# Kernel optimization log

Hardware: AMD Instinct MI355X
Metric: run time of the kernel (lower is better)

The kernel has to match this reference:

```python
import jax, jax.numpy as jnp
import numpy as np

N = 100000        # nodes
E_HALF = 1600000  # directed edges before symmetrization
NFEAT, NHID, NOUT = 512, 256, 64
K = 10            # Chebyshev order


def setup_inputs() -> dict:
    key = jax.random.key(0)
    k_feat, k_src, k_dst, k_w1, k_w2, k_tmp = jax.random.split(key, 6)
    feature = jax.random.normal(k_feat, (N, NFEAT), jnp.float32)
    src = jax.random.randint(k_src, (E_HALF,), 0, N, jnp.int32)
    dst = jax.random.randint(k_dst, (E_HALF,), 0, N, jnp.int32)
    # symmetrize so the adjacency (and hence the normalized Laplacian) is symmetric
    edge_index = jnp.stack([jnp.concatenate([src, dst]), jnp.concatenate([dst, src])])  # [2, 2*E_HALF]
    W1 = jax.random.normal(k_w1, (NHID, NFEAT), jnp.float32) / np.sqrt(NFEAT)
    b1 = jnp.zeros((NHID,), jnp.float32)
    W2 = jax.random.normal(k_w2, (NOUT, NHID), jnp.float32) / np.sqrt(NHID)
    b2 = jnp.zeros((NOUT,), jnp.float32)
    # ChebnetII_prop.temp is initialized to 1.0; jitter so relu/grads are non-trivial
    temp = 1.0 + 0.1 * jax.random.normal(k_tmp, (K + 1,), jnp.float32)
    return {"feature": feature, "W1": W1, "b1": b1, "W2": W2, "b2": b2,
            "temp": temp, "edge_index": edge_index}


def _cheb_coeffs(temp):
    # coe[i] = 2/(K+1) * sum_j relu(temp)[j] * T_i(x_j),  x_j = cos((K-j+0.5)*pi/(K+1))
    # and T_i(cos(theta)) = cos(i*theta)
    coe_tmp = jax.nn.relu(temp)
    j = jnp.arange(K + 1, dtype=temp.dtype)
    theta = (K - j + 0.5) * jnp.pi / (K + 1)          # [K+1]
    i = jnp.arange(K + 1, dtype=temp.dtype)
    T = jnp.cos(i[:, None] * theta[None, :])           # [K+1, K+1] Chebyshev eval table
    return (2.0 / (K + 1)) * (T @ coe_tmp)             # [K+1]


def reference(feature, W1, b1, W2, b2, temp, edge_index):
    # dense MLP part (dropout is identity in eval mode)
    x = jax.nn.relu(feature @ W1.T + b1)               # [N, NHID]
    x = x @ W2.T + b2                                  # [N, NOUT]

    # ChebnetII_prop: propagate with L_tilde = L_sym - I = -D^{-1/2} A D^{-1/2}
    row, col = edge_index[0], edge_index[1]
    w = jnp.ones(row.shape, x.dtype)                   # unit edge weights (binary adjacency)
    deg = jax.ops.segment_sum(w, row, num_segments=N)  # [N]
    dinv = jnp.where(deg > 0, jax.lax.rsqrt(jnp.maximum(deg, 1.0)), 0.0)
    norm = -dinv[row] * w * dinv[col]                  # [E] edge weights of (L - I)

    def prop(v):  # v: [N, NOUT] -> (L - I) @ v via gather/scatter
        return jax.ops.segment_sum(norm[:, None] * v[col], row, num_segments=N)

    coe = _cheb_coeffs(temp)
    Tx0 = x
    Tx1 = prop(x)
    out = coe[0] / 2.0 * Tx0 + coe[1] * Tx1
    for i in range(2, K + 1):                          # Chebyshev recursion (K fixed, small)
        Tx2 = 2.0 * prop(Tx1) - Tx0
        out = out + coe[i] * Tx2
        Tx0, Tx1 = Tx1, Tx2
    return out                                         # [N, NOUT]
```

## Files before the change

kernel.cpp:

```cpp
#include <hip/hip_runtime.h>

#define K_ORDER 10
#define NFEAT 512
#define NHID 256
#define NOUT 64
#define PI_F 3.14159265358979323846f
#define SCAN_CHUNK 2048

typedef __bf16 bf16x8 __attribute__((ext_vector_type(8)));
typedef unsigned short ushort8 __attribute__((ext_vector_type(8)));
typedef float f32x4 __attribute__((ext_vector_type(4)));

__device__ __forceinline__ float bf2f(unsigned short u) {
    union { unsigned int i; float f; } x;
    x.i = ((unsigned int)u) << 16;
    return x.f;
}

__global__ void detect_kernel(const unsigned short* __restrict__ temp, int* __restrict__ flag) {
    if (threadIdx.x == 0 && blockIdx.x == 0) {
        int cnt = 0;
        for (int i = 0; i < K_ORDER + 1; ++i) {
            unsigned short s = temp[i];
            if (s >= 0x3E00 && s < 0x4080) cnt++;
        }
        flag[0] = (cnt >= 9) ? 1 : 0;
    }
}


__global__ void count_deg_kernel(const int* __restrict__ row, int* __restrict__ deg, int e) {
    int i = blockIdx.x * blockDim.x + threadIdx.x;
    if (i < e) atomicAdd(&deg[row[i]], 1);
}

__global__ void dinv_kernel(const int* __restrict__ deg, float* __restrict__ dinv, int n) {
    int i = blockIdx.x * blockDim.x + threadIdx.x;
    if (i < n) {
        int d = deg[i];
        dinv[i] = (d > 0) ? rsqrtf((float)d) : 0.0f;
    }
}


__global__ __launch_bounds__(256) void partial_sum_kernel(const int* __restrict__ deg,
                                                          int* __restrict__ bsum, int n) {
    __shared__ int ws[4];
    int b = blockIdx.x, t = threadIdx.x;
    int base = b * SCAN_CHUNK + t * 8;
    int s = 0;
    #pragma unroll
    for (int j = 0; j < 8; ++j) { int i = base + j; if (i < n) s += deg[i]; }
    #pragma unroll
    for (int m = 1; m < 64; m <<= 1) s += __shfl_xor(s, m, 64);
    if ((t & 63) == 0) ws[t >> 6] = s;
    __syncthreads();
    if (t == 0) bsum[b] = ws[0] + ws[1] + ws[2] + ws[3];
}

__global__ void scan_small_kernel(const int* __restrict__ bsum, int* __restrict__ boff,
                                  int* __restrict__ rowptr, int nb, int n) {
    int t = threadIdx.x;
    int v = (t < nb) ? bsum[t] : 0;
    int x = v;
    #pragma unroll
    for (int m = 1; m < 64; m <<= 1) { int y = __shfl_up(x, m, 64); if (t >= m) x += y; }
    if (t < nb) boff[t] = x - v;
    if (t == 63) rowptr[n] = x;
}

__global__ __launch_bounds__(256) void scan_apply_kernel(const int* __restrict__ deg,
                                                         const int* __restrict__ boff,
                                                         int* __restrict__ rowptr,
                                                         int* __restrict__ cursor, int n) {
    __shared__ int wtot[4];
    __shared__ int woff_s[4];
    int b = blockIdx.x, t = threadIdx.x;
    int lane = t & 63, wid = t >> 6;
    int base = b * SCAN_CHUNK + t * 8;
    int v[8], s[8];
    int run = 0;
    #pragma unroll
    for (int j = 0; j < 8; ++j) {
        int i = base + j;
        v[j] = (i < n) ? deg[i] : 0;
        run += v[j];
        s[j] = run;
    }
    int tsum = run;
    int x = tsum;
    #pragma unroll
    for (int m = 1; m < 64; m <<= 1) { int y = __shfl_up(x, m, 64); if (lane >= m) x += y; }
    int texcl = x - tsum;
    if (lane == 63) wtot[wid] = x;
    __syncthreads();
    if (t == 0) {
        int r = 0;
        #pragma unroll
        for (int w = 0; w < 4; ++w) { woff_s[w] = r; r += wtot[w]; }
    }
    __syncthreads();
    int ebase = boff[b] + woff_s[wid] + texcl;
    #pragma unroll
    for (int j = 0; j < 8; ++j) {
        int i = base + j;
        if (i < n) { int ex = ebase + s[j] - v[j]; rowptr[i] = ex; cursor[i] = ex; }
    }
}

__global__ void scatter_kernel(const int* __restrict__ row, const int* __restrict__ col,
                               int* __restrict__ cursor, int* __restrict__ cols_s, int e) {
    int i = blockIdx.x * blockDim.x + threadIdx.x;
    if (i < e) {
        int p = atomicAdd(&cursor[row[i]], 1);
        cols_s[p] = col[i];
    }
}


__global__ void coef_kernel(const void* __restrict__ temp, const int* __restrict__ flag,
                            float* __restrict__ coe) {
    int i = threadIdx.x;
    bool isbf = flag[0] != 0;
    if (i <= K_ORDER) {
        float s = 0.0f;
        #pragma unroll
        for (int j = 0; j <= K_ORDER; ++j) {
            float t = isbf ? bf2f(((const unsigned short*)temp)[j]) : ((const float*)temp)[j];
            t = fmaxf(t, 0.0f);
            float theta = ((float)(K_ORDER - j) + 0.5f) * PI_F / (float)(K_ORDER + 1);
            s += cosf((float)i * theta) * t;
        }
        coe[i] = (2.0f / (float)(K_ORDER + 1)) * s;
    }
}


template<int BN, bool RELU, bool A_FLAGGED>
__global__ __launch_bounds__(256) void gemm_kernel(const void* __restrict__ A,
                                                   const void* __restrict__ B,
                                                   const void* __restrict__ bias,
                                                   const int* __restrict__ flag,
                                                   unsigned short* __restrict__ C,
                                                   int M, int Kdim, int ldc) {
    constexpr int BM = 128, BK = 32;
    constexpr int FN = BN / 32;
    constexpr int LDT = BK + 8;
    __shared__ unsigned short lds_a[BM * LDT] __attribute__((aligned(16)));
    __shared__ unsigned short lds_b[BN * LDT] __attribute__((aligned(16)));

    const bool isbf = flag[0] != 0;
    int tid = threadIdx.x;
    int lane = tid & 63, wid = tid >> 6;
    int row0 = blockIdx.x * BM;
    int col0 = blockIdx.y * BN;
    int wrow = (wid >> 1) * (BM / 2);
    int wcol = (wid & 1) * (BN / 2);

    f32x4 acc[4][FN] = {};

    for (int k0 = 0; k0 < Kdim; k0 += BK) {
        #pragma unroll
        for (int it = 0; it < (BM * BK / 8) / 256; ++it) {
            int idx = it * 256 + tid;
            int r = idx >> 2;
            int kc = (idx & 3) * 8;
            int gr = row0 + r; if (gr >= M) gr = M - 1;
            size_t base = (size_t)gr * Kdim + k0 + kc;
            if (!A_FLAGGED || isbf) {
                *(ushort8*)&lds_a[r * LDT + kc] = *(const ushort8*)((const unsigned short*)A + base);
            } else {
                const float* Af = (const float*)A;
                f32x4 lo = *(const f32x4*)(Af + base);
                f32x4 hi = *(const f32x4*)(Af + base + 4);
                bf16x8 v;
                #pragma unroll
                for (int j = 0; j < 4; ++j) { v[j] = (__bf16)lo[j]; v[j + 4] = (__bf16)hi[j]; }
                *(bf16x8*)&lds_a[r * LDT + kc] = v;
            }
        }
        #pragma unroll
        for (int it = 0; it < (BN * BK / 8) / 256; ++it) {
            int idx = it * 256 + tid;
            int r = idx >> 2;
            int kc = (idx & 3) * 8;
            size_t base = (size_t)(col0 + r) * Kdim + k0 + kc;
            if (isbf) {
                *(ushort8*)&lds_b[r * LDT + kc] = *(const ushort8*)((const unsigned short*)B + base);
            } else {
                const float* Bf = (const float*)B;
                f32x4 lo = *(const f32x4*)(Bf + base);
                f32x4 hi = *(const f32x4*)(Bf + base + 4);
                bf16x8 v;
                #pragma unroll
                for (int j = 0; j < 4; ++j) { v[j] = (__bf16)lo[j]; v[j + 4] = (__bf16)hi[j]; }
                *(bf16x8*)&lds_b[r * LDT + kc] = v;
            }
        }
        __syncthreads();

        int kq = (lane >> 4) * 8;
        bf16x8 af[4];
        bf16x8 bfr[FN];
        #pragma unroll
        for (int mi = 0; mi < 4; ++mi)
            af[mi] = *(bf16x8*)&lds_a[(wrow + mi * 16 + (lane & 15)) * LDT + kq];
        #pragma unroll
        for (int ni = 0; ni < FN; ++ni)
            bfr[ni] = *(bf16x8*)&lds_b[(wcol + ni * 16 + (lane & 15)) * LDT + kq];
        #pragma unroll
        for (int mi = 0; mi < 4; ++mi)
            #pragma unroll
            for (int ni = 0; ni < FN; ++ni)
                acc[mi][ni] = __builtin_amdgcn_mfma_f32_16x16x32_bf16(af[mi], bfr[ni],
                                                                      acc[mi][ni], 0, 0, 0);
        __syncthreads();
    }

    #pragma unroll
    for (int mi = 0; mi < 4; ++mi) {
        #pragma unroll
        for (int ni = 0; ni < FN; ++ni) {
            #pragma unroll
            for (int rg = 0; rg < 4; ++rg) {
                int grow = row0 + wrow + mi * 16 + (lane >> 4) * 4 + rg;
                int gcol = col0 + wcol + ni * 16 + (lane & 15);
                if (grow < M) {
                    float bb = isbf ? bf2f(((const unsigned short*)bias)[gcol])
                                    : ((const float*)bias)[gcol];
                    float vv = acc[mi][ni][rg] + bb;
                    if (RELU) vv = fmaxf(vv, 0.0f);
                    __bf16 h = (__bf16)vv;
                    C[(size_t)grow * ldc + gcol] = *(unsigned short*)&h;
                }
            }
        }
    }
}


__global__ __launch_bounds__(256) void prop_kernel(const unsigned short* __restrict__ vsrc,
                                                   unsigned short* __restrict__ tdst,
                                                   float* __restrict__ outacc,
                                                   const int* __restrict__ rowptr,
                                                   const int* __restrict__ cols,
                                                   const float* __restrict__ dinv,
                                                   const float* __restrict__ coe,
                                                   int mode, int ci, int n) {
    int lane = threadIdx.x & 63;
    int r = blockIdx.x * 4 + (threadIdx.x >> 6);
    if (r >= n) return;
    int fc = lane & 7;
    int sub = lane >> 3;
    int e0 = rowptr[r], e1 = rowptr[r + 1];
    float acc[8] = {};
    for (int e = e0; e < e1; e += 8) {
        int ee = e + sub;
        bool valid = ee < e1;
        int c = valid ? cols[ee] : 0;
        float w = valid ? dinv[c] : 0.0f;
        ushort8 vv = *(const ushort8*)&vsrc[(size_t)c * NOUT + fc * 8];
        #pragma unroll
        for (int j = 0; j < 8; ++j)
            acc[j] = fmaf(w, bf2f(vv[j]), acc[j]);
    }
    #pragma unroll
    for (int m = 8; m < 64; m <<= 1)
        #pragma unroll
        for (int j = 0; j < 8; ++j)
            acc[j] += __shfl_xor(acc[j], m, 64);

    if (lane < 8) {
        float dr = -dinv[r];
        size_t idx = (size_t)r * NOUT + lane * 8;
        float P[8];
        #pragma unroll
        for (int j = 0; j < 8; ++j) P[j] = dr * acc[j];
        if (mode == 0) {
            ushort8 v0 = *(const ushort8*)&vsrc[idx];
            ushort8 hout;
            #pragma unroll
            for (int j = 0; j < 8; ++j) {
                __bf16 h = (__bf16)P[j];
                hout[j] = *(unsigned short*)&h;
            }
            *(ushort8*)&tdst[idx] = hout;
            #pragma unroll
            for (int j = 0; j < 8; ++j)
                outacc[idx + j] = coe[0] * 0.5f * bf2f(v0[j]) + coe[1] * P[j];
        } else {
            ushort8 t0v = *(const ushort8*)&tdst[idx];
            ushort8 hout;
            float t2a[8];
            #pragma unroll
            for (int j = 0; j < 8; ++j) {
                float t2 = 2.0f * P[j] - bf2f(t0v[j]);
                t2a[j] = t2;
                __bf16 h = (__bf16)t2;
                hout[j] = *(unsigned short*)&h;
            }
            *(ushort8*)&tdst[idx] = hout;
            #pragma unroll
            for (int j = 0; j < 8; ++j)
                outacc[idx + j] += coe[ci] * t2a[j];
        }
    }
}

__global__ void convert_kernel(const float* __restrict__ in, const int* __restrict__ flag,
                               void* __restrict__ out, int n) {
    int i = blockIdx.x * blockDim.x + threadIdx.x;
    bool isbf = flag[0] != 0;
    if (i < n) {
        float v = in[i];
        if (isbf) {
            __bf16 h = (__bf16)v;
            ((unsigned short*)out)[i] = *(unsigned short*)&h;
        } else {
            ((float*)out)[i] = v;
        }
    }
}


extern "C" void kernel_launch(void* const* d_in, const int* in_sizes, int n_in,
                              void* d_out, int out_size, void* d_ws, size_t ws_size,
                              hipStream_t stream) {
    const void* feature = d_in[0];
    const void* W1      = d_in[1];
    const void* b1      = d_in[2];
    const void* W2      = d_in[3];
    const void* b2      = d_in[4];
    const void* temp    = d_in[5];
    const int* edge_index = (const int*)d_in[6];

    const int N = in_sizes[0] / NFEAT;
    const int E = in_sizes[6] / 2;
    const int* row = edge_index;
    const int* col = edge_index + E;
    const int nb = (N + SCAN_CHUNK - 1) / SCAN_CHUNK;

    char* base = (char*)d_ws;
    size_t off = 0;
    auto alloc = [&](size_t bytes) -> char* {
        char* p = base + off;
        off = (off + bytes + 255) & ~(size_t)255;
        return p;
    };
    int*   flag   = (int*)  alloc(4);
    float* coe    = (float*)alloc(64);
    int*   bsum   = (int*)  alloc(256);
    int*   boff   = (int*)  alloc(256);
    float* dinv   = (float*)alloc((size_t)N * 4);
    int*   deg    = (int*)  alloc((size_t)N * 4);
    int*   rowptr = (int*)  alloc((size_t)(N + 1) * 4);
    int*   cursor = (int*)  alloc((size_t)(N + 1) * 4);
    char*  R      = alloc((size_t)N * NHID * 2);
    unsigned short* xhid = (unsigned short*)R;
    int*   colss  = (int*)R;
    float* outacc = (float*)(R + (size_t)E * 4);
    unsigned short* t_a = (unsigned short*)alloc((size_t)N * NOUT * 2);
    unsigned short* t_b = (unsigned short*)alloc((size_t)N * NOUT * 2);

    detect_kernel<<<1, 64, 0, stream>>>((const unsigned short*)temp, flag);
    coef_kernel<<<1, 64, 0, stream>>>(temp, flag, coe);

    gemm_kernel<128, true, true><<<dim3((N + 127) / 128, NHID / 128), 256, 0, stream>>>(
        feature, W1, b1, flag, xhid, N, NFEAT, NHID);
    gemm_kernel<64, false, false><<<dim3((N + 127) / 128, 1), 256, 0, stream>>>(
        xhid, W2, b2, flag, t_a, N, NHID, NOUT);

    hipMemsetAsync(deg, 0, (size_t)N * 4, stream);
    count_deg_kernel<<<(E + 255) / 256, 256, 0, stream>>>(row, deg, E);
    dinv_kernel<<<(N + 255) / 256, 256, 0, stream>>>(deg, dinv, N);
    partial_sum_kernel<<<nb, 256, 0, stream>>>(deg, bsum, N);
    scan_small_kernel<<<1, 64, 0, stream>>>(bsum, boff, rowptr, nb, N);
    scan_apply_kernel<<<nb, 256, 0, stream>>>(deg, boff, rowptr, cursor, N);
    scatter_kernel<<<(E + 255) / 256, 256, 0, stream>>>(row, col, cursor, colss, E);

    int pb = (N + 3) / 4;
    prop_kernel<<<pb, 256, 0, stream>>>(t_a, t_b, outacc, rowptr, colss, dinv, coe, 0, 0, N);
    unsigned short* src = t_b;
    unsigned short* dst = t_a;
    for (int i = 2; i <= K_ORDER; ++i) {
        prop_kernel<<<pb, 256, 0, stream>>>(src, dst, outacc, rowptr, colss, dinv, coe, 1, i, N);
        unsigned short* tmp = src; src = dst; dst = tmp;
    }

    convert_kernel<<<(N * NOUT + 255) / 256, 256, 0, stream>>>(outacc, flag, d_out, N * NOUT);
}
```

Measured before the change: 1.562 ms.

## Two-pass binned CSR scatter to improve write locality

Replaces the single random-access CSR scatter with two passes. The first pass bins edges by row>>4 into a pair buffer using bucket cursors; the second does the per-row atomic scatter from that partially sorted buffer. The aim is to make the scatter's atomics and column writes more local and cache friendly. The cost is an extra pass over the edges and an 8-byte-per-edge intermediate buffer stored in the reused region.

```diff
diff --git a/kernel.cpp b/kernel.cpp
--- a/kernel.cpp
+++ b/kernel.cpp
@@ -6,6 +6,7 @@
 #define NOUT 64
 #define PI_F 3.14159265358979323846f
 #define SCAN_CHUNK 2048
+#define BSHIFT 4
 
 typedef __bf16 bf16x8 __attribute__((ext_vector_type(8)));
 typedef unsigned short ushort8 __attribute__((ext_vector_type(8)));
@@ -108,12 +109,30 @@
     }
 }
 
-__global__ void scatter_kernel(const int* __restrict__ row, const int* __restrict__ col,
-                               int* __restrict__ cursor, int* __restrict__ cols_s, int e) {
+
+__global__ void init_bcur_kernel(const int* __restrict__ rowptr, int* __restrict__ bcur, int nbk) {
+    int b = blockIdx.x * blockDim.x + threadIdx.x;
+    if (b < nbk) bcur[b] = rowptr[b << BSHIFT];
+}
+
+__global__ void bin_kernel(const int* __restrict__ row, const int* __restrict__ col,
+                           int* __restrict__ bcur, int2* __restrict__ pairbuf, int e) {
     int i = blockIdx.x * blockDim.x + threadIdx.x;
     if (i < e) {
-        int p = atomicAdd(&cursor[row[i]], 1);
-        cols_s[p] = col[i];
+        int r = row[i];
+        int c = col[i];
+        int p = atomicAdd(&bcur[r >> BSHIFT], 1);
+        pairbuf[p] = make_int2(r, c);
+    }
+}
+
+__global__ void scatter2_kernel(const int2* __restrict__ pairbuf, int* __restrict__ cursor,
+                                int* __restrict__ cols_s, int e) {
+    int i = blockIdx.x * blockDim.x + threadIdx.x;
+    if (i < e) {
+        int2 pr = pairbuf[i];
+        int p = atomicAdd(&cursor[pr.x], 1);
+        cols_s[p] = pr.y;
     }
 }
 
@@ -339,6 +358,7 @@
     const int* row = edge_index;
     const int* col = edge_index + E;
     const int nb = (N + SCAN_CHUNK - 1) / SCAN_CHUNK;
+    const int nbk = (N + (1 << BSHIFT) - 1) >> BSHIFT;
 
     char* base = (char*)d_ws;
     size_t off = 0;
@@ -351,6 +371,7 @@
     float* coe    = (float*)alloc(64);
     int*   bsum   = (int*)  alloc(256);
     int*   boff   = (int*)  alloc(256);
+    int*   bcur   = (int*)  alloc((size_t)nbk * 4);
     float* dinv   = (float*)alloc((size_t)N * 4);
     int*   deg    = (int*)  alloc((size_t)N * 4);
     int*   rowptr = (int*)  alloc((size_t)(N + 1) * 4);
@@ -358,6 +379,7 @@
     char*  R      = alloc((size_t)N * NHID * 2);
     unsigned short* xhid = (unsigned short*)R;
     int*   colss  = (int*)R;
+    int2*  pairbuf = (int2*)(R + (size_t)E * 4);
     float* outacc = (float*)(R + (size_t)E * 4);
     unsigned short* t_a = (unsigned short*)alloc((size_t)N * NOUT * 2);
     unsigned short* t_b = (unsigned short*)alloc((size_t)N * NOUT * 2);
@@ -376,7 +398,9 @@
     partial_sum_kernel<<<nb, 256, 0, stream>>>(deg, bsum, N);
     scan_small_kernel<<<1, 64, 0, stream>>>(bsum, boff, rowptr, nb, N);
     scan_apply_kernel<<<nb, 256, 0, stream>>>(deg, boff, rowptr, cursor, N);
-    scatter_kernel<<<(E + 255) / 256, 256, 0, stream>>>(row, col, cursor, colss, E);
+    init_bcur_kernel<<<(nbk + 255) / 256, 256, 0, stream>>>(rowptr, bcur, nbk);
+    bin_kernel<<<(E + 255) / 256, 256, 0, stream>>>(row, col, bcur, pairbuf, E);
+    scatter2_kernel<<<(E + 255) / 256, 256, 0, stream>>>(pairbuf, cursor, colss, E);
 
     int pb = (N + 3) / 4;
     prop_kernel<<<pb, 256, 0, stream>>>(t_a, t_b, outacc, rowptr, colss, dinv, coe, 0, 0, N);
```

Measured after the change: 1.594 ms. 1.02x slower.

## Double-buffer GEMM with direct global-to-LDS loads and pre-converted bf16 weights

Applied to the files above, without the earlier changes.

Rewrites the dense GEMM kernels to stage tiles into double-buffered LDS with async global_load_lds, using XOR swizzles instead of padded rows. When the activations arrive as fp32, the conversion to bf16 moves to fragment-load time. A new prep kernel converts the weights and biases to bf16 and fp32 once per call, and the grid is flattened so both column tiles of a row block are adjacent for L2 reuse of A. The goal is to overlap the next tile's loads with MFMA work and cut conversion and register staging overhead. The fp32 path doubles the LDS footprint, and the swizzle indexing has to match exactly or results will be wrong.

```diff
diff --git a/kernel.cpp b/kernel.cpp
--- a/kernel.cpp
+++ b/kernel.cpp
@@ -17,6 +17,15 @@
     return x.f;
 }
 
+__device__ __forceinline__ unsigned short f2bfu(float f) {
+    __bf16 h = (__bf16)f;
+    return *(unsigned short*)&h;
+}
+
+#define GLOAD_LDS16(g, l) __builtin_amdgcn_global_load_lds( \
+    (const __attribute__((address_space(1))) void*)(g),     \
+    (__attribute__((address_space(3))) void*)(l), 16, 0, 0)
+
 __global__ void detect_kernel(const unsigned short* __restrict__ temp, int* __restrict__ flag) {
     if (threadIdx.x == 0 && blockIdx.x == 0) {
         int cnt = 0;
@@ -28,6 +37,26 @@
     }
 }
 
+__global__ void prep_weights(const void* __restrict__ W1, const void* __restrict__ b1,
+                             const void* __restrict__ W2, const void* __restrict__ b2,
+                             const int* __restrict__ flag,
+                             unsigned short* __restrict__ w1o, float* __restrict__ b1o,
+                             unsigned short* __restrict__ w2o, float* __restrict__ b2o) {
+    bool isbf = flag[0] != 0;
+    int stride = gridDim.x * blockDim.x;
+    int i0 = blockIdx.x * blockDim.x + threadIdx.x;
+    const int n1 = NHID * NFEAT;
+    const int n2 = NOUT * NHID;
+    for (int i = i0; i < n1; i += stride)
+        w1o[i] = isbf ? ((const unsigned short*)W1)[i] : f2bfu(((const float*)W1)[i]);
+    for (int i = i0; i < n2; i += stride)
+        w2o[i] = isbf ? ((const unsigned short*)W2)[i] : f2bfu(((const float*)W2)[i]);
+    for (int i = i0; i < NHID; i += stride)
+        b1o[i] = isbf ? bf2f(((const unsigned short*)b1)[i]) : ((const float*)b1)[i];
+    for (int i = i0; i < NOUT; i += stride)
+        b2o[i] = isbf ? bf2f(((const unsigned short*)b2)[i]) : ((const float*)b2)[i];
+}
+
 
 __global__ void count_deg_kernel(const int* __restrict__ row, int* __restrict__ deg, int e) {
     int i = blockIdx.x * blockDim.x + threadIdx.x;
@@ -41,7 +70,6 @@
         dinv[i] = (d > 0) ? rsqrtf((float)d) : 0.0f;
     }
 }
-
 
 __global__ __launch_bounds__(256) void partial_sum_kernel(const int* __restrict__ deg,
                                                           int* __restrict__ bsum, int n) {
@@ -136,85 +164,120 @@
 }
 
 
-template<int BN, bool RELU, bool A_FLAGGED>
-__global__ __launch_bounds__(256) void gemm_kernel(const void* __restrict__ A,
-                                                   const void* __restrict__ B,
-                                                   const void* __restrict__ bias,
-                                                   const int* __restrict__ flag,
-                                                   unsigned short* __restrict__ C,
-                                                   int M, int Kdim, int ldc) {
+template<int BN, int NBY, bool RELU, bool A_FLAGGED>
+__global__ __launch_bounds__(256) void gemm_kernel(
+    const void* __restrict__ A, const unsigned short* __restrict__ Bw,
+    const float* __restrict__ bias, const int* __restrict__ flag,
+    unsigned short* __restrict__ C, int M, int Kdim, int ldc)
+{
     constexpr int BM = 128, BK = 32;
     constexpr int FN = BN / 32;
-    constexpr int LDT = BK + 8;
-    __shared__ unsigned short lds_a[BM * LDT] __attribute__((aligned(16)));
-    __shared__ unsigned short lds_b[BN * LDT] __attribute__((aligned(16)));
-
-    const bool isbf = flag[0] != 0;
-    int tid = threadIdx.x;
-    int lane = tid & 63, wid = tid >> 6;
-    int row0 = blockIdx.x * BM;
-    int col0 = blockIdx.y * BN;
-    int wrow = (wid >> 1) * (BM / 2);
-    int wcol = (wid & 1) * (BN / 2);
+    constexpr int ABUF = A_FLAGGED ? (BM * BK * 4) : (BM * BK * 2);
+    constexpr int BBUF = BN * BK * 2;
+    __shared__ char lds[2 * ABUF + 2 * BBUF] __attribute__((aligned(16)));
+
+    const int tid = threadIdx.x;
+    const int lane = tid & 63, wid = tid >> 6;
+    const int bid = blockIdx.x;
+    const int by = bid % NBY;
+    const int bx = bid / NBY;
+    const int row0 = bx * BM;
+    const int col0 = by * BN;
+    const int wrow = (wid >> 1) * (BM / 2);
+    const int wcol = (wid & 1) * (BN / 2);
+    const bool af32 = A_FLAGGED ? (flag[0] == 0) : false;
+
+    char* ldsA0 = lds;
+    char* ldsB0 = lds + 2 * ABUF;
+
+    auto stage = [&](int buf, int k0) {
+        {
+            constexpr int PW = (BBUF / 1024) / 4;
+            #pragma unroll
+            for (int rr = 0; rr < PW; ++rr) {
+                int q = rr * 4 + wid;
+                int off = q * 1024 + lane * 16;
+                int brow = off >> 6;
+                int scol = ((off >> 4) & 3) ^ (brow & 3);
+                const char* src = (const char*)Bw + (((size_t)(col0 + brow) * Kdim + k0) << 1) + scol * 16;
+                GLOAD_LDS16(src, ldsB0 + buf * BBUF + q * 1024);
+            }
+        }
+        if (af32) {
+            #pragma unroll
+            for (int rr = 0; rr < 4; ++rr) {
+                int q = rr * 4 + wid;
+                int off = q * 1024 + lane * 16;
+                int arow = off >> 7;
+                int scol = ((off >> 4) & 7) ^ (arow & 7);
+                int grow = row0 + arow; if (grow >= M) grow = M - 1;
+                const char* src = (const char*)A + (((size_t)grow * Kdim + k0) << 2) + scol * 16;
+                GLOAD_LDS16(src, ldsA0 + buf * ABUF + q * 1024);
+            }
+        } else {
+            #pragma unroll
+            for (int rr = 0; rr < 2; ++rr) {
+                int q = rr * 4 + wid;
+                int off = q * 1024 + lane * 16;
+                int arow = off >> 6;
+                int scol = ((off >> 4) & 3) ^ (arow & 3);
+                int grow = row0 + arow; if (grow >= M) grow = M - 1;
+                const char* src = (const char*)A + (((size_t)grow * Kdim + k0) << 1) + scol * 16;
+                GLOAD_LDS16(src, ldsA0 + buf * ABUF + q * 1024);
+            }
+        }
+    };
 
     f32x4 acc[4][FN] = {};
 
-    for (int k0 = 0; k0 < Kdim; k0 += BK) {
-        #pragma unroll
-        for (int it = 0; it < (BM * BK / 8) / 256; ++it) {
-            int idx = it * 256 + tid;
-            int r = idx >> 2;
-            int kc = (idx & 3) * 8;
-            int gr = row0 + r; if (gr >= M) gr = M - 1;
-            size_t base = (size_t)gr * Kdim + k0 + kc;
-            if (!A_FLAGGED || isbf) {
-                *(ushort8*)&lds_a[r * LDT + kc] = *(const ushort8*)((const unsigned short*)A + base);
-            } else {
-                const float* Af = (const float*)A;
-                f32x4 lo = *(const f32x4*)(Af + base);
-                f32x4 hi = *(const f32x4*)(Af + base + 4);
-                bf16x8 v;
+    auto compute = [&](int buf) {
+        const char* Ab = ldsA0 + buf * ABUF;
+        const char* Bb = ldsB0 + buf * BBUF;
+        const int kq = lane >> 4;
+        bf16x8 af[4];
+        if (af32) {
+            #pragma unroll
+            for (int mi = 0; mi < 4; ++mi) {
+                int aRow = wrow + mi * 16 + (lane & 15);
+                int base = aRow * 128 + kq * 32;
+                int sw = (aRow & 7) << 4;
+                f32x4 lo = *(const f32x4*)(Ab + (base ^ sw));
+                f32x4 hi = *(const f32x4*)(Ab + ((base + 16) ^ sw));
                 #pragma unroll
-                for (int j = 0; j < 4; ++j) { v[j] = (__bf16)lo[j]; v[j + 4] = (__bf16)hi[j]; }
-                *(bf16x8*)&lds_a[r * LDT + kc] = v;
-            }
-        }
-        #pragma unroll
-        for (int it = 0; it < (BN * BK / 8) / 256; ++it) {
-            int idx = it * 256 + tid;
-            int r = idx >> 2;
-            int kc = (idx & 3) * 8;
-            size_t base = (size_t)(col0 + r) * Kdim + k0 + kc;
-            if (isbf) {
-                *(ushort8*)&lds_b[r * LDT + kc] = *(const ushort8*)((const unsigned short*)B + base);
-            } else {
-                const float* Bf = (const float*)B;
-                f32x4 lo = *(const f32x4*)(Bf + base);
-                f32x4 hi = *(const f32x4*)(Bf + base + 4);
-                bf16x8 v;
-                #pragma unroll
-                for (int j = 0; j < 4; ++j) { v[j] = (__bf16)lo[j]; v[j + 4] = (__bf16)hi[j]; }
-                *(bf16x8*)&lds_b[r * LDT + kc] = v;
-            }
-        }
+                for (int j = 0; j < 4; ++j) { af[mi][j] = (__bf16)lo[j]; af[mi][j + 4] = (__bf16)hi[j]; }
+            }
+        } else {
+            #pragma unroll
+            for (int mi = 0; mi < 4; ++mi) {
+                int aRow = wrow + mi * 16 + (lane & 15);
+                int o = (aRow * 64 + kq * 16) ^ ((aRow & 3) << 4);
+                af[mi] = *(const bf16x8*)(Ab + o);
+            }
+        }
+        bf16x8 bfv[FN];
+        #pragma unroll
+        for (int ni = 0; ni < FN; ++ni) {
+            int bRow = wcol + ni * 16 + (lane & 15);
+            int o = (bRow * 64 + kq * 16) ^ ((bRow & 3) << 4);
+            bfv[ni] = *(const bf16x8*)(Bb + o);
+        }
+        #pragma unroll
+        for (int mi = 0; mi < 4; ++mi)
+            #pragma unroll
+            for (int ni = 0; ni < FN; ++ni)
+                acc[mi][ni] = __builtin_amdgcn_mfma_f32_16x16x32_bf16(af[mi], bfv[ni],
+                                                                      acc[mi][ni], 0, 0, 0);
+    };
+
+    const int NT = Kdim / BK;
+    stage(0, 0);
+    __syncthreads();
+    int buf = 0;
+    for (int t = 0; t < NT; ++t) {
+        if (t + 1 < NT) stage(buf ^ 1, (t + 1) * BK);
+        compute(buf);
         __syncthreads();
-
-        int kq = (lane >> 4) * 8;
-        bf16x8 af[4];
-        bf16x8 bfr[FN];
-        #pragma unroll
-        for (int mi = 0; mi < 4; ++mi)
-            af[mi] = *(bf16x8*)&lds_a[(wrow + mi * 16 + (lane & 15)) * LDT + kq];
-        #pragma unroll
-        for (int ni = 0; ni < FN; ++ni)
-            bfr[ni] = *(bf16x8*)&lds_b[(wcol + ni * 16 + (lane & 15)) * LDT + kq];
-        #pragma unroll
-        for (int mi = 0; mi < 4; ++mi)
-            #pragma unroll
-            for (int ni = 0; ni < FN; ++ni)
-                acc[mi][ni] = __builtin_amdgcn_mfma_f32_16x16x32_bf16(af[mi], bfr[ni],
-                                                                      acc[mi][ni], 0, 0, 0);
-        __syncthreads();
+        buf ^= 1;
     }
 
     #pragma unroll
@@ -226,12 +289,9 @@
                 int grow = row0 + wrow + mi * 16 + (lane >> 4) * 4 + rg;
                 int gcol = col0 + wcol + ni * 16 + (lane & 15);
                 if (grow < M) {
-                    float bb = isbf ? bf2f(((const unsigned short*)bias)[gcol])
-                                    : ((const float*)bias)[gcol];
-                    float vv = acc[mi][ni][rg] + bb;
+                    float vv = acc[mi][ni][rg] + bias[gcol];
                     if (RELU) vv = fmaxf(vv, 0.0f);
-                    __bf16 h = (__bf16)vv;
-                    C[(size_t)grow * ldc + gcol] = *(unsigned short*)&h;
+                    C[(size_t)grow * ldc + gcol] = f2bfu(vv);
                 }
             }
         }
@@ -351,6 +411,10 @@
     float* coe    = (float*)alloc(64);
     int*   bsum   = (int*)  alloc(256);
     int*   boff   = (int*)  alloc(256);
+    unsigned short* w1c = (unsigned short*)alloc((size_t)NHID * NFEAT * 2);
+    float* b1c    = (float*)alloc(NHID * 4);
+    unsigned short* w2c = (unsigned short*)alloc((size_t)NOUT * NHID * 2);
+    float* b2c    = (float*)alloc(NOUT * 4);
     float* dinv   = (float*)alloc((size_t)N * 4);
     int*   deg    = (int*)  alloc((size_t)N * 4);
     int*   rowptr = (int*)  alloc((size_t)(N + 1) * 4);
@@ -364,11 +428,13 @@
 
     detect_kernel<<<1, 64, 0, stream>>>((const unsigned short*)temp, flag);
     coef_kernel<<<1, 64, 0, stream>>>(temp, flag, coe);
-
-    gemm_kernel<128, true, true><<<dim3((N + 127) / 128, NHID / 128), 256, 0, stream>>>(
-        feature, W1, b1, flag, xhid, N, NFEAT, NHID);
-    gemm_kernel<64, false, false><<<dim3((N + 127) / 128, 1), 256, 0, stream>>>(
-        xhid, W2, b2, flag, t_a, N, NHID, NOUT);
+    prep_weights<<<128, 256, 0, stream>>>(W1, b1, W2, b2, flag, w1c, b1c, w2c, b2c);
+
+    const int nbm = (N + 127) / 128;
+    gemm_kernel<128, 2, true, true><<<dim3(nbm * 2), 256, 0, stream>>>(
+        feature, w1c, b1c, flag, xhid, N, NFEAT, NHID);
+    gemm_kernel<64, 1, false, false><<<dim3(nbm), 256, 0, stream>>>(
+        xhid, w2c, b2c, flag, t_a, N, NHID, NOUT);
 
     hipMemsetAsync(deg, 0, (size_t)N * 4, stream);
     count_deg_kernel<<<(E + 255) / 256, 256, 0, stream>>>(row, deg, E);
```

Measured after the change: 1.542 ms. About the same (-1.3%).
